# Kernel tuning notes

Hardware: AMD Instinct MI355X
Metric: run time of the kernel (lower is better)

The kernel has to match this reference:

```python
import jax, jax.numpy as jnp
import numpy as np

NEG_SLOPE = 0.2  # PyG GATv2Conv default leaky_relu negative slope


def _gatv2_layer(x, src, dst, n, Wl, bl, Wr, br, att, bias, concat):
    # PyG GATv2Conv (share_weights=False, edge_dim=None):
    #   x_l = lin_l(x) on source, x_r = lin_r(x) on target
    #   m = leaky_relu(x_l[src] + x_r[dst]); alpha = softmax_dst(<m, att>)
    #   out[i] = sum_{e: dst=i} alpha_e * x_l[src_e]
    H, C = att.shape
    xl = (x @ Wl + bl).reshape(n, H, C)
    xr = (x @ Wr + br).reshape(n, H, C)
    m = jax.nn.leaky_relu(xl[src] + xr[dst], NEG_SLOPE)      # [E,H,C]
    logits = jnp.einsum('ehc,hc->eh', m, att)                # [E,H]
    lmax = jax.ops.segment_max(logits, dst, num_segments=n)  # [N,H]
    e = jnp.exp(logits - lmax[dst])
    denom = jax.ops.segment_sum(e, dst, num_segments=n)
    alpha = e / (denom[dst] + 1e-16)                         # [E,H]
    out = jax.ops.segment_sum(xl[src] * alpha[:, :, None], dst, num_segments=n)
    out = out.reshape(n, H * C) if concat else out.mean(axis=1)
    return out + bias


def _glorot(key, shape):
    fan_in, fan_out = shape[0], shape[-1]
    s = jnp.sqrt(6.0 / (fan_in + fan_out))
    return jax.random.uniform(key, shape, jnp.float32, -s, s)


def setup_inputs() -> dict:
    key = jax.random.key(0)
    N, E, B = 50000, 800000, 512
    node_in, hidden, heads, meta_dim = 128, 32, 4, 12
    ks = jax.random.split(key, 32)
    inp = {
        'x': jax.random.normal(ks[0], (N, node_in), jnp.float32),
        'edge_index': jax.random.randint(ks[1], (2, E), 0, N, jnp.int64),
        'batch': jnp.sort(jax.random.randint(ks[2], (N,), 0, B, jnp.int64)),
        'metadata': jax.random.normal(ks[3], (B, meta_dim), jnp.float32),
    }
    dims = [(node_in, hidden, heads), (hidden * heads, hidden, heads), (hidden * heads, hidden, 1)]
    i = 4
    for li, (din, dh, H) in enumerate(dims):
        inp[f'Wl{li}'] = _glorot(ks[i], (din, H * dh)); i += 1
        inp[f'bl{li}'] = jnp.zeros((H * dh,), jnp.float32)
        inp[f'Wr{li}'] = _glorot(ks[i], (din, H * dh)); i += 1
        inp[f'br{li}'] = jnp.zeros((H * dh,), jnp.float32)
        inp[f'att{li}'] = _glorot(ks[i], (H, dh)); i += 1
        out_dim = H * dh if li < 2 else dh  # last layer concat=False
        inp[f'b{li}'] = jnp.zeros((out_dim,), jnp.float32)
    pool_dim = hidden  # n_layers=3 -> final single-head layer
    inp['Wh1'] = _glorot(ks[i], (pool_dim + meta_dim, pool_dim)); i += 1
    inp['bh1'] = jnp.zeros((pool_dim,), jnp.float32)
    inp['Wh2'] = _glorot(ks[i], (pool_dim, 1)); i += 1
    inp['bh2'] = jnp.zeros((1,), jnp.float32)
    return inp


def reference(x, edge_index, batch, metadata,
              Wl0, bl0, Wr0, br0, att0, b0,
              Wl1, bl1, Wr1, br1, att1, b1,
              Wl2, bl2, Wr2, br2, att2, b2,
              Wh1, bh1, Wh2, bh2):
    n = x.shape[0]
    B = metadata.shape[0]
    # PyG GATv2Conv add_self_loops=True
    loop = jnp.arange(n, dtype=edge_index.dtype)
    src = jnp.concatenate([edge_index[0], loop])
    dst = jnp.concatenate([edge_index[1], loop])
    params = [(Wl0, bl0, Wr0, br0, att0, b0, True),
              (Wl1, bl1, Wr1, br1, att1, b1, True),
              (Wl2, bl2, Wr2, br2, att2, b2, False)]
    h = x
    for (Wl, bl, Wr, br, att, bias, concat) in params:
        h = _gatv2_layer(h, src, dst, n, Wl, bl, Wr, br, att, bias, concat)
        h = jax.nn.elu(h)  # dropout is identity in eval mode
    # global mean pool over graphs
    sums = jax.ops.segment_sum(h, batch, num_segments=B)
    cnt = jax.ops.segment_sum(jnp.ones((n,), h.dtype), batch, num_segments=B)
    emb = sums / jnp.clip(cnt, 1.0)[:, None]
    z = jnp.concatenate([emb, metadata], axis=1)
    z = jax.nn.relu(z @ Wh1 + bh1)
    return z @ Wh2 + bh2  # (B, 1) logits
```

## Files before the change

### kernel.cpp

```cpp
#include <hip/hip_runtime.h>
#include <cstdint>
#include <cstddef>

#define NEG_SLOPE 0.2f
#define LOG2E 1.44269504f
#define NBLK 256

typedef __attribute__((ext_vector_type(8))) short short8;
typedef __attribute__((ext_vector_type(4))) float f32x4;

__device__ __forceinline__ float bf2f(unsigned short u) {
    union { unsigned int i; float f; } x; x.i = ((unsigned int)u) << 16; return x.f;
}
__device__ __forceinline__ unsigned short f2bf(float f) {
    union { float f; unsigned int i; } x;
    x.f = f;
    unsigned int u = x.i;
    return (unsigned short)((u + 0x7FFFu + ((u >> 16) & 1u)) >> 16);
}

__device__ __forceinline__ float dpp_sum8(float p) {
    p += __int_as_float(__builtin_amdgcn_update_dpp(0, __float_as_int(p), 0xB1, 0xF, 0xF, true));
    p += __int_as_float(__builtin_amdgcn_update_dpp(0, __float_as_int(p), 0x4E, 0xF, 0xF, true));
    p += __int_as_float(__builtin_amdgcn_update_dpp(0, __float_as_int(p), 0x141, 0xF, 0xF, true));
    return p;
}

__global__ __launch_bounds__(256) void prep_w_all(
    const float* __restrict__ Wl0, const float* __restrict__ Wr0,
    const float* __restrict__ Wl1, const float* __restrict__ Wr1,
    const float* __restrict__ Wl2, const float* __restrict__ Wr2,
    unsigned short* __restrict__ Bt0, unsigned short* __restrict__ Bt1,
    unsigned short* __restrict__ Bt2)
{
    int idx = blockIdx.x * 256 + threadIdx.x;
    const int SZ = 256 * 128;
    const float *Wl, *Wr; unsigned short* Bt; int dout;
    if (idx < SZ)              { Wl = Wl0; Wr = Wr0; Bt = Bt0; dout = 128; }
    else if (idx < 2 * SZ)     { Wl = Wl1; Wr = Wr1; Bt = Bt1; dout = 128; idx -= SZ; }
    else if (idx < 2 * SZ + 64 * 128) { Wl = Wl2; Wr = Wr2; Bt = Bt2; dout = 32; idx -= 2 * SZ; }
    else return;
    int n = idx >> 7, k = idx & 127;
    float v = (n < dout) ? Wl[(size_t)k * dout + n] : Wr[(size_t)k * dout + (n - dout)];
    Bt[idx] = f2bf(v);
}

template<int BN, bool ABF16>
__global__ __launch_bounds__(256) void gemm_mfma(
    const void* __restrict__ Avoid, int M,
    const unsigned short* __restrict__ Bt,
    const float* __restrict__ bl, const float* __restrict__ br,
    int dout, unsigned short* __restrict__ XL, unsigned short* __restrict__ XR)
{
    constexpr int LDA = 136;
    constexpr int NT  = BN / 16;
    __shared__ __attribute__((aligned(16))) unsigned short Bs[BN * LDA];
    const int t  = threadIdx.x;
    const int m0 = blockIdx.x * 64;
    const int n0 = blockIdx.y * BN;

    const int w    = t >> 6;
    const int lane = t & 63;
    const int fr   = lane & 15;
    const int quad = lane >> 4;

#pragma unroll
    for (int i = 0; i < BN / 16; ++i) {
        int c  = t + i * 256;
        int n  = c >> 4;
        int kc = (c & 15) * 8;
        *(short8*)(Bs + n * LDA + kc) =
            *(const short8*)(Bt + (size_t)(n0 + n) * 128 + kc);
    }

    const int arow = m0 + w * 16 + fr;
    const size_t abase = (size_t)(arow < M ? arow : 0) * 128 + quad * 8;
    short8 afr[4];
    if (ABF16) {
        const unsigned short* A = (const unsigned short*)Avoid;
#pragma unroll
        for (int kk = 0; kk < 4; ++kk)
            afr[kk] = *(const short8*)(A + abase + kk * 32);
    } else {
        const float* A = (const float*)Avoid;
#pragma unroll
        for (int kk = 0; kk < 4; ++kk) {
            float4 lo = *(const float4*)(A + abase + kk * 32);
            float4 hi = *(const float4*)(A + abase + kk * 32 + 4);
            afr[kk][0] = (short)f2bf(lo.x); afr[kk][1] = (short)f2bf(lo.y);
            afr[kk][2] = (short)f2bf(lo.z); afr[kk][3] = (short)f2bf(lo.w);
            afr[kk][4] = (short)f2bf(hi.x); afr[kk][5] = (short)f2bf(hi.y);
            afr[kk][6] = (short)f2bf(hi.z); afr[kk][7] = (short)f2bf(hi.w);
        }
    }
    __syncthreads();

    f32x4 acc[NT] = {};
    const unsigned short* bp = Bs + fr * LDA + quad * 8;
#pragma unroll
    for (int kk = 0; kk < 4; ++kk) {
#pragma unroll
        for (int j = 0; j < NT; ++j) {
            short8 bfr = *(const short8*)(bp + j * 16 * LDA + kk * 32);
            acc[j] = __builtin_amdgcn_mfma_f32_16x16x32_bf16(afr[kk], bfr, acc[j], 0, 0, 0);
        }
    }

#pragma unroll
    for (int j = 0; j < NT; ++j) {
        int col = n0 + j * 16 + fr;
        float bias = (col < dout) ? bl[col] : br[col - dout];
#pragma unroll
        for (int r = 0; r < 4; ++r) {
            int row = m0 + w * 16 + quad * 4 + r;
            if (row < M) {
                unsigned short o = f2bf(acc[j][r] + bias);
                if (col < dout) XL[(size_t)row * dout + col] = o;
                else            XR[(size_t)row * dout + (col - dout)] = o;
            }
        }
    }
}

__global__ __launch_bounds__(256) void csr_hist(
    const int* __restrict__ dst, int E, int tile, int* __restrict__ hist)
{
    __shared__ int h[256];
    const int t = threadIdx.x, b = blockIdx.x;
    h[t] = 0;
    __syncthreads();
    const int e0 = b * tile;
    const int e1 = min(E, e0 + tile);
    for (int e = e0 + t; e < e1; e += 256)
        atomicAdd(&h[dst[e] >> 8], 1);
    __syncthreads();
    hist[t * NBLK + b] = h[t];
}

__global__ __launch_bounds__(256) void csr_scatter(
    const int* __restrict__ src, const int* __restrict__ dst, int E, int tile,
    const int* __restrict__ hist_s, unsigned int* __restrict__ sorted)
{
    __shared__ int cur[256];
    const int t = threadIdx.x, b = blockIdx.x;
    cur[t] = hist_s[t * NBLK + b];
    __syncthreads();
    const int e0 = b * tile;
    const int e1 = min(E, e0 + tile);
    for (int e = e0 + t; e < e1; e += 256) {
        int d = dst[e];
        int pos = atomicAdd(&cur[d >> 8], 1);
        sorted[pos] = ((unsigned int)d << 16) | (unsigned int)src[e];
    }
}

__global__ __launch_bounds__(256) void csr_fine(
    const unsigned int* __restrict__ sorted, int E, int N,
    const int* __restrict__ hist_s,
    int* __restrict__ rowptr, unsigned short* __restrict__ csr_src)
{
    __shared__ int h[256];
    __shared__ int sc[256];
    const int t = threadIdx.x, d = blockIdx.x;
    const int start = hist_s[d * NBLK];
    const int end   = (d < 255) ? hist_s[(d + 1) * NBLK] : E;
    h[t] = 0;
    __syncthreads();
    for (int e = start + t; e < end; e += 256)
        atomicAdd(&h[(sorted[e] >> 16) & 0xFF], 1);
    __syncthreads();
    int v = h[t];
    sc[t] = v;
    __syncthreads();
    for (int off = 1; off < 256; off <<= 1) {
        int u = (t >= off) ? sc[t - off] : 0;
        __syncthreads();
        sc[t] += u;
        __syncthreads();
    }
    const int base = start + sc[t] - v;
    const int node = (d << 8) + t;
    if (node <= N) rowptr[node] = base;
    h[t] = base;
    __syncthreads();
    for (int e = start + t; e < end; e += 256) {
        unsigned int it = sorted[e];
        int pos = atomicAdd(&h[(it >> 16) & 0xFF], 1);
        csr_src[pos] = (unsigned short)(it & 0xFFFFu);
    }
}

__global__ __launch_bounds__(256) void scan_partial(
    const int* __restrict__ cnt, int N, int* __restrict__ bsum)
{
    __shared__ int red[4];
    const int t = threadIdx.x;
    const int base = blockIdx.x * 2048;
    int s = 0;
#pragma unroll
    for (int i = 0; i < 8; ++i) {
        int idx = base + t + i * 256;
        if (idx < N) s += cnt[idx];
    }
#pragma unroll
    for (int off = 32; off >= 1; off >>= 1) s += __shfl_xor(s, off);
    if ((t & 63) == 0) red[t >> 6] = s;
    __syncthreads();
    if (t == 0) bsum[blockIdx.x] = red[0] + red[1] + red[2] + red[3];
}

__global__ __launch_bounds__(256) void scan_bsums(
    int* __restrict__ bsum, int nb, int E, int* __restrict__ rowptr, int N)
{
    __shared__ int sh[256];
    const int t = threadIdx.x;
    int v = (t < nb) ? bsum[t] : 0;
    sh[t] = v;
    __syncthreads();
    for (int off = 1; off < 256; off <<= 1) {
        int u = (t >= off) ? sh[t - off] : 0;
        __syncthreads();
        sh[t] += u;
        __syncthreads();
    }
    if (t < nb) bsum[t] = sh[t] - v;
    if (t == 0) rowptr[N] = E;
}

__global__ __launch_bounds__(256) void scan_final(
    const int* __restrict__ cnt, int N, const int* __restrict__ bsum,
    int* __restrict__ rowptr)
{
    __shared__ int sdat[2048];
    __shared__ int tsum[256];
    const int t = threadIdx.x;
    const int base = blockIdx.x * 2048;
#pragma unroll
    for (int i = 0; i < 8; ++i) {
        int idx = base + t + i * 256;
        sdat[t + i * 256] = (idx < N) ? cnt[idx] : 0;
    }
    __syncthreads();
    int vals[8];
    int s = 0;
#pragma unroll
    for (int j = 0; j < 8; ++j) { vals[j] = sdat[t * 8 + j]; s += vals[j]; }
    tsum[t] = s;
    __syncthreads();
    for (int off = 1; off < 256; off <<= 1) {
        int u = (t >= off) ? tsum[t - off] : 0;
        __syncthreads();
        tsum[t] += u;
        __syncthreads();
    }
    int run = bsum[blockIdx.x] + tsum[t] - s;
#pragma unroll
    for (int j = 0; j < 8; ++j) { sdat[t * 8 + j] = run; run += vals[j]; }
    __syncthreads();
#pragma unroll
    for (int i = 0; i < 8; ++i) {
        int idx = base + t + i * 256;
        if (idx < N) rowptr[idx] = sdat[t + i * 256];
    }
}

template<int H>
__global__ __launch_bounds__(256, 4) void gat_fused(
    const unsigned short* __restrict__ xl, const unsigned short* __restrict__ xr,
    const int* __restrict__ rowptr, const unsigned short* __restrict__ csr_src,
    const float* __restrict__ att, const float* __restrict__ bias,
    unsigned short* __restrict__ hout, int hstride, int N)
{
    constexpr int HC  = 32 * H;
    constexpr int LPE = HC / 4;
    constexpr int EPW = 64 / LPE;
    const int node = blockIdx.x * 4 + (threadIdx.x >> 6);
    if (node >= N) return;
    const int lane = threadIdx.x & 63;
    const int q    = lane % LPE;
    const int slot = lane / LPE;
    const int rs   = rowptr[node];
    const int re   = rowptr[node + 1];

    const unsigned short* __restrict__ xlb = xl + 4 * q;
    float4 xri;
    {
        ushort4 u = *(const ushort4*)(xr + (size_t)node * HC + 4 * q);
        xri.x = bf2f(u.x); xri.y = bf2f(u.y); xri.z = bf2f(u.z); xri.w = bf2f(u.w);
    }
    float4 b1, b2;
    {
        float4 a = *(const float4*)(att + 4 * q);
        const float c1 = 0.5f * (1.0f + NEG_SLOPE) * LOG2E;
        const float c2 = 0.5f * (1.0f - NEG_SLOPE) * LOG2E;
        b1.x = a.x * c1; b1.y = a.y * c1; b1.z = a.z * c1; b1.w = a.w * c1;
        b2.x = a.x * c2; b2.y = a.y * c2; b2.z = a.z * c2; b2.w = a.w * c2;
    }

    float l = 0.f;
    float4 acc = make_float4(0.f, 0.f, 0.f, 0.f);

    auto ld4 = [&](int s) -> float4 {
        ushort4 u = *(const ushort4*)(xlb + (size_t)s * HC);
        float4 v;
        v.x = bf2f(u.x); v.y = bf2f(u.y); v.z = bf2f(u.z); v.w = bf2f(u.w);
        return v;
    };

    auto edge_w = [&](const float4& v) -> float {
        float sx = v.x + xri.x, sy = v.y + xri.y, sz = v.z + xri.z, sw = v.w + xri.w;
        float p  = b1.x * sx;
        float pq = b2.x * fabsf(sx);
        p  = fmaf(b1.y, sy, p);
        pq = fmaf(b2.y, fabsf(sy), pq);
        p  = fmaf(b1.z, sz, p);
        pq = fmaf(b2.z, fabsf(sz), pq);
        p  = fmaf(b1.w, sw, p);
        pq = fmaf(b2.w, fabsf(sw), pq);
        p += pq;
        p = dpp_sum8(p);
        return exp2f(p);
    };

    if (slot == 0) {
        float4 v = ld4(node);
        float w = edge_w(v);
        l = w;
        acc.x = w * v.x; acc.y = w * v.y; acc.z = w * v.z; acc.w = w * v.w;
    }

    int k = rs + slot;
    for (; k + EPW < re; k += 2 * EPW) {
        int s0 = csr_src[k];
        int s1 = csr_src[k + EPW];
        float4 v0 = ld4(s0);
        float4 v1 = ld4(s1);
        float w0 = edge_w(v0);
        float w1 = edge_w(v1);
        l += w0 + w1;
        acc.x = fmaf(w0, v0.x, fmaf(w1, v1.x, acc.x));
        acc.y = fmaf(w0, v0.y, fmaf(w1, v1.y, acc.y));
        acc.z = fmaf(w0, v0.z, fmaf(w1, v1.z, acc.z));
        acc.w = fmaf(w0, v0.w, fmaf(w1, v1.w, acc.w));
    }
    if (k < re) {
        int s0 = csr_src[k];
        float4 v0 = ld4(s0);
        float w0 = edge_w(v0);
        l += w0;
        acc.x = fmaf(w0, v0.x, acc.x);
        acc.y = fmaf(w0, v0.y, acc.y);
        acc.z = fmaf(w0, v0.z, acc.z);
        acc.w = fmaf(w0, v0.w, acc.w);
    }

#pragma unroll
    for (int mask = LPE; mask < 64; mask <<= 1) {
        l     += __shfl_xor(l, mask);
        acc.x += __shfl_xor(acc.x, mask);
        acc.y += __shfl_xor(acc.y, mask);
        acc.z += __shfl_xor(acc.z, mask);
        acc.w += __shfl_xor(acc.w, mask);
    }

    if (lane < LPE) {
        const float4 bi = *(const float4*)(bias + 4 * q);
        float inv = 1.f / (l + 1e-16f);
        float4 o;
        o.x = acc.x * inv + bi.x;
        o.y = acc.y * inv + bi.y;
        o.z = acc.z * inv + bi.z;
        o.w = acc.w * inv + bi.w;
        o.x = (o.x > 0.f) ? o.x : expm1f(o.x);
        o.y = (o.y > 0.f) ? o.y : expm1f(o.y);
        o.z = (o.z > 0.f) ? o.z : expm1f(o.z);
        o.w = (o.w > 0.f) ? o.w : expm1f(o.w);
        ushort4 ob;
        ob.x = f2bf(o.x); ob.y = f2bf(o.y); ob.z = f2bf(o.z); ob.w = f2bf(o.w);
        *(ushort4*)(hout + (size_t)node * hstride + 4 * q) = ob;
    }
}

__global__ __launch_bounds__(128) void pool_head_kernel(
    const unsigned short* __restrict__ h, int hstride,
    const int* __restrict__ batch, int N,
    const float* __restrict__ meta,
    const float* __restrict__ Wh1, const float* __restrict__ bh1,
    const float* __restrict__ Wh2, const float* __restrict__ bh2,
    float* __restrict__ out)
{
    const int b = blockIdx.x;
    const int t = threadIdx.x;
    __shared__ float s[128];
    __shared__ float z[44];

    int lo = 0, hi = N;
    while (lo < hi) { int mid = (lo + hi) >> 1; if (batch[mid] < b) lo = mid + 1; else hi = mid; }
    int lo2 = lo, hi2 = N;
    while (lo2 < hi2) { int mid = (lo2 + hi2) >> 1; if (batch[mid] < b + 1) lo2 = mid + 1; else hi2 = mid; }
    const int start = lo, end = lo2;

    const int c = t & 31, r = t >> 5;
    float acc = 0.f;
    for (int row = start + r; row < end; row += 4)
        acc += bf2f(h[(size_t)row * hstride + c]);
    s[t] = acc;
    __syncthreads();
    if (t < 32) {
        float sum = s[t] + s[t + 32] + s[t + 64] + s[t + 96];
        z[t] = sum / fmaxf((float)(end - start), 1.0f);
    } else if (t < 44) {
        z[t] = meta[(size_t)b * 12 + (t - 32)];
    }
    __syncthreads();
    if (t < 32) {
        float hj = bh1[t];
#pragma unroll
        for (int k = 0; k < 44; ++k)
            hj = fmaf(z[k], Wh1[k * 32 + t], hj);
        hj = fmaxf(hj, 0.f);
        float p = hj * Wh2[t];
#pragma unroll
        for (int off = 16; off >= 1; off >>= 1)
            p += __shfl_xor(p, off, 32);
        if (t == 0) out[b] = p + bh2[0];
    }
}

extern "C" void kernel_launch(void* const* d_in, const int* in_sizes, int n_in,
                              void* d_out, int out_size, void* d_ws, size_t ws_size,
                              hipStream_t stream)
{
    const float* x     = (const float*)d_in[0];
    const int*   ei    = (const int*)d_in[1];
    const int*   batch = (const int*)d_in[2];
    const float* meta  = (const float*)d_in[3];
    const float* Wl[3]  = {(const float*)d_in[4],  (const float*)d_in[10], (const float*)d_in[16]};
    const float* bl[3]  = {(const float*)d_in[5],  (const float*)d_in[11], (const float*)d_in[17]};
    const float* Wr[3]  = {(const float*)d_in[6],  (const float*)d_in[12], (const float*)d_in[18]};
    const float* br[3]  = {(const float*)d_in[7],  (const float*)d_in[13], (const float*)d_in[19]};
    const float* att[3] = {(const float*)d_in[8],  (const float*)d_in[14], (const float*)d_in[20]};
    const float* bb[3]  = {(const float*)d_in[9],  (const float*)d_in[15], (const float*)d_in[21]};
    const float* Wh1 = (const float*)d_in[22];
    const float* bh1 = (const float*)d_in[23];
    const float* Wh2 = (const float*)d_in[24];
    const float* bh2 = (const float*)d_in[25];
    float* out = (float*)d_out;

    const int N  = in_sizes[0] / 128;
    const int E  = in_sizes[1] / 2;
    const int B  = in_sizes[3] / 12;

    char* wsp = (char*)d_ws;
    size_t off_ = 0;
    auto alloc = [&](size_t bytes) {
        char* p = wsp + off_;
        off_ = (off_ + bytes + 255) & ~(size_t)255;
        return p;
    };
    unsigned short* xlbuf = (unsigned short*)alloc((size_t)N * 128 * 2);
    unsigned short* xrbuf = (unsigned short*)alloc((size_t)N * 128 * 2);
    unsigned short* hbuf  = (unsigned short*)alloc((size_t)N * 128 * 2);
    int*   rowptr  = (int*)alloc((size_t)(N + 1) * 4);
    unsigned short* csr_src = (unsigned short*)alloc((size_t)E * 2);
    unsigned int*   sorted  = (unsigned int*)alloc((size_t)E * 4);
    int*   hist_g  = (int*)alloc((size_t)65536 * 4);
    int*   hist_s  = (int*)alloc((size_t)65537 * 4);
    unsigned short* Bt0     = (unsigned short*)alloc((size_t)256 * 128 * 2);
    unsigned short* Bt1     = (unsigned short*)alloc((size_t)256 * 128 * 2);
    unsigned short* Bt2     = (unsigned short*)alloc((size_t)64 * 128 * 2);
    int*   bsum    = (int*)alloc((size_t)256 * 4);

    const int* srcI = ei;
    const int* dstI = ei + E;

    prep_w_all<<<(2 * 256 * 128 + 64 * 128 + 255) / 256, 256, 0, stream>>>(
        Wl[0], Wr[0], Wl[1], Wr[1], Wl[2], Wr[2], Bt0, Bt1, Bt2);

    const int tile = (E + NBLK - 1) / NBLK;
    csr_hist<<<NBLK, 256, 0, stream>>>(dstI, E, tile, hist_g);
    scan_partial<<<32, 256, 0, stream>>>(hist_g, 65536, bsum);
    scan_bsums<<<1, 256, 0, stream>>>(bsum, 32, E, hist_s, 65536);
    scan_final<<<32, 256, 0, stream>>>(hist_g, 65536, bsum, hist_s);
    csr_scatter<<<NBLK, 256, 0, stream>>>(srcI, dstI, E, tile, hist_s, sorted);
    csr_fine<<<(N >> 8) + 1, 256, 0, stream>>>(sorted, E, N, hist_s, rowptr, csr_src);

    const int GB = (N + 3) / 4;
    const int MB = (N + 63) / 64;

    {
        gemm_mfma<128, false><<<dim3(MB, 2), 256, 0, stream>>>(x, N, Bt0, bl[0], br[0], 128, xlbuf, xrbuf);
        gat_fused<4><<<GB, 256, 0, stream>>>(xlbuf, xrbuf, rowptr, csr_src, att[0], bb[0], hbuf, 128, N);
    }
    {
        gemm_mfma<128, true><<<dim3(MB, 2), 256, 0, stream>>>(hbuf, N, Bt1, bl[1], br[1], 128, xlbuf, xrbuf);
        gat_fused<4><<<GB, 256, 0, stream>>>(xlbuf, xrbuf, rowptr, csr_src, att[1], bb[1], hbuf, 128, N);
    }
    {
        gemm_mfma<64, true><<<dim3(MB, 1), 256, 0, stream>>>(hbuf, N, Bt2, bl[2], br[2], 32, xlbuf, xrbuf);
        gat_fused<1><<<GB, 256, 0, stream>>>(xlbuf, xrbuf, rowptr, csr_src, att[2], bb[2], hbuf, 32, N);
    }
    pool_head_kernel<<<B, 128, 0, stream>>>(hbuf, 32, batch, N, meta, Wh1, bh1, Wh2, bh2, out);
}
```

Baseline: 340.8 us.

## Fuse weight prep with histogram, single-block scan, split GAT launches in halves

```diff
diff --git a/kernel.cpp b/kernel.cpp
--- a/kernel.cpp
+++ b/kernel.cpp
@@ -26,14 +26,28 @@
     return p;
 }
 
-__global__ __launch_bounds__(256) void prep_w_all(
+__global__ __launch_bounds__(256) void prep_and_hist(
     const float* __restrict__ Wl0, const float* __restrict__ Wr0,
     const float* __restrict__ Wl1, const float* __restrict__ Wr1,
     const float* __restrict__ Wl2, const float* __restrict__ Wr2,
     unsigned short* __restrict__ Bt0, unsigned short* __restrict__ Bt1,
-    unsigned short* __restrict__ Bt2)
-{
-    int idx = blockIdx.x * 256 + threadIdx.x;
+    unsigned short* __restrict__ Bt2,
+    const int* __restrict__ dst, int E, int tile, int* __restrict__ hist)
+{
+    __shared__ int h[256];
+    const int t = threadIdx.x;
+    const int b = blockIdx.x;
+    if (b < NBLK) {
+        h[t] = 0;
+        __syncthreads();
+        const int e0 = b * tile;
+        const int e1 = min(E, e0 + tile);
+        for (int e = e0 + t; e < e1; e += 256)
+            atomicAdd(&h[dst[e] >> 8], 1);
+        __syncthreads();
+        hist[t * NBLK + b] = h[t];
+    }
+    int idx = b * 256 + t;
     const int SZ = 256 * 128;
     const float *Wl, *Wr; unsigned short* Bt; int dout;
     if (idx < SZ)              { Wl = Wl0; Wr = Wr0; Bt = Bt0; dout = 128; }
@@ -45,6 +59,34 @@
     Bt[idx] = f2bf(v);
 }
 
+__global__ __launch_bounds__(1024) void scan_one(
+    const int* __restrict__ g, int* __restrict__ s_out)
+{
+    __shared__ int wsum[16];
+    const int t = threadIdx.x;
+    int vals[64];
+    int tot = 0;
+#pragma unroll
+    for (int i = 0; i < 64; ++i) { vals[i] = g[t * 64 + i]; tot += vals[i]; }
+    int s = tot;
+#pragma unroll
+    for (int off = 1; off < 64; off <<= 1) {
+        int u = __shfl_up(s, off);
+        if ((t & 63) >= off) s += u;
+    }
+    if ((t & 63) == 63) wsum[t >> 6] = s;
+    __syncthreads();
+    if (t == 0) {
+        int run = 0;
+#pragma unroll
+        for (int i = 0; i < 16; ++i) { int v = wsum[i]; wsum[i] = run; run += v; }
+    }
+    __syncthreads();
+    int run = wsum[t >> 6] + s - tot;
+#pragma unroll
+    for (int i = 0; i < 64; ++i) { s_out[t * 64 + i] = run; run += vals[i]; }
+}
+
 template<int BN, bool ABF16>
 __global__ __launch_bounds__(256) void gemm_mfma(
     const void* __restrict__ Avoid, int M,
@@ -122,21 +164,6 @@
     }
 }
 
-__global__ __launch_bounds__(256) void csr_hist(
-    const int* __restrict__ dst, int E, int tile, int* __restrict__ hist)
-{
-    __shared__ int h[256];
-    const int t = threadIdx.x, b = blockIdx.x;
-    h[t] = 0;
-    __syncthreads();
-    const int e0 = b * tile;
-    const int e1 = min(E, e0 + tile);
-    for (int e = e0 + t; e < e1; e += 256)
-        atomicAdd(&h[dst[e] >> 8], 1);
-    __syncthreads();
-    hist[t * NBLK + b] = h[t];
-}
-
 __global__ __launch_bounds__(256) void csr_scatter(
     const int* __restrict__ src, const int* __restrict__ dst, int E, int tile,
     const int* __restrict__ hist_s, unsigned int* __restrict__ sorted)
@@ -190,92 +217,18 @@
     }
 }
 
-__global__ __launch_bounds__(256) void scan_partial(
-    const int* __restrict__ cnt, int N, int* __restrict__ bsum)
-{
-    __shared__ int red[4];
-    const int t = threadIdx.x;
-    const int base = blockIdx.x * 2048;
-    int s = 0;
-#pragma unroll
-    for (int i = 0; i < 8; ++i) {
-        int idx = base + t + i * 256;
-        if (idx < N) s += cnt[idx];
-    }
-#pragma unroll
-    for (int off = 32; off >= 1; off >>= 1) s += __shfl_xor(s, off);
-    if ((t & 63) == 0) red[t >> 6] = s;
-    __syncthreads();
-    if (t == 0) bsum[blockIdx.x] = red[0] + red[1] + red[2] + red[3];
-}
-
-__global__ __launch_bounds__(256) void scan_bsums(
-    int* __restrict__ bsum, int nb, int E, int* __restrict__ rowptr, int N)
-{
-    __shared__ int sh[256];
-    const int t = threadIdx.x;
-    int v = (t < nb) ? bsum[t] : 0;
-    sh[t] = v;
-    __syncthreads();
-    for (int off = 1; off < 256; off <<= 1) {
-        int u = (t >= off) ? sh[t - off] : 0;
-        __syncthreads();
-        sh[t] += u;
-        __syncthreads();
-    }
-    if (t < nb) bsum[t] = sh[t] - v;
-    if (t == 0) rowptr[N] = E;
-}
-
-__global__ __launch_bounds__(256) void scan_final(
-    const int* __restrict__ cnt, int N, const int* __restrict__ bsum,
-    int* __restrict__ rowptr)
-{
-    __shared__ int sdat[2048];
-    __shared__ int tsum[256];
-    const int t = threadIdx.x;
-    const int base = blockIdx.x * 2048;
-#pragma unroll
-    for (int i = 0; i < 8; ++i) {
-        int idx = base + t + i * 256;
-        sdat[t + i * 256] = (idx < N) ? cnt[idx] : 0;
-    }
-    __syncthreads();
-    int vals[8];
-    int s = 0;
-#pragma unroll
-    for (int j = 0; j < 8; ++j) { vals[j] = sdat[t * 8 + j]; s += vals[j]; }
-    tsum[t] = s;
-    __syncthreads();
-    for (int off = 1; off < 256; off <<= 1) {
-        int u = (t >= off) ? tsum[t - off] : 0;
-        __syncthreads();
-        tsum[t] += u;
-        __syncthreads();
-    }
-    int run = bsum[blockIdx.x] + tsum[t] - s;
-#pragma unroll
-    for (int j = 0; j < 8; ++j) { sdat[t * 8 + j] = run; run += vals[j]; }
-    __syncthreads();
-#pragma unroll
-    for (int i = 0; i < 8; ++i) {
-        int idx = base + t + i * 256;
-        if (idx < N) rowptr[idx] = sdat[t + i * 256];
-    }
-}
-
 template<int H>
 __global__ __launch_bounds__(256, 4) void gat_fused(
     const unsigned short* __restrict__ xl, const unsigned short* __restrict__ xr,
     const int* __restrict__ rowptr, const unsigned short* __restrict__ csr_src,
     const float* __restrict__ att, const float* __restrict__ bias,
-    unsigned short* __restrict__ hout, int hstride, int N)
+    unsigned short* __restrict__ hout, int hstride, int node0, int nodeEnd)
 {
     constexpr int HC  = 32 * H;
     constexpr int LPE = HC / 4;
     constexpr int EPW = 64 / LPE;
-    const int node = blockIdx.x * 4 + (threadIdx.x >> 6);
-    if (node >= N) return;
+    const int node = node0 + blockIdx.x * 4 + (threadIdx.x >> 6);
+    if (node >= nodeEnd) return;
     const int lane = threadIdx.x & 63;
     const int q    = lane % LPE;
     const int slot = lane / LPE;
@@ -469,36 +422,39 @@
     unsigned short* Bt0     = (unsigned short*)alloc((size_t)256 * 128 * 2);
     unsigned short* Bt1     = (unsigned short*)alloc((size_t)256 * 128 * 2);
     unsigned short* Bt2     = (unsigned short*)alloc((size_t)64 * 128 * 2);
-    int*   bsum    = (int*)alloc((size_t)256 * 4);
 
     const int* srcI = ei;
     const int* dstI = ei + E;
 
-    prep_w_all<<<(2 * 256 * 128 + 64 * 128 + 255) / 256, 256, 0, stream>>>(
-        Wl[0], Wr[0], Wl[1], Wr[1], Wl[2], Wr[2], Bt0, Bt1, Bt2);
-
     const int tile = (E + NBLK - 1) / NBLK;
-    csr_hist<<<NBLK, 256, 0, stream>>>(dstI, E, tile, hist_g);
-    scan_partial<<<32, 256, 0, stream>>>(hist_g, 65536, bsum);
-    scan_bsums<<<1, 256, 0, stream>>>(bsum, 32, E, hist_s, 65536);
-    scan_final<<<32, 256, 0, stream>>>(hist_g, 65536, bsum, hist_s);
+    prep_and_hist<<<288, 256, 0, stream>>>(
+        Wl[0], Wr[0], Wl[1], Wr[1], Wl[2], Wr[2], Bt0, Bt1, Bt2,
+        dstI, E, tile, hist_g);
+
+    scan_one<<<1, 1024, 0, stream>>>(hist_g, hist_s);
+
     csr_scatter<<<NBLK, 256, 0, stream>>>(srcI, dstI, E, tile, hist_s, sorted);
     csr_fine<<<(N >> 8) + 1, 256, 0, stream>>>(sorted, E, N, hist_s, rowptr, csr_src);
 
-    const int GB = (N + 3) / 4;
     const int MB = (N + 63) / 64;
+    const int half = (N + 1) / 2;
+    const int GB1 = (half + 3) / 4;
+    const int GB2 = (N - half + 3) / 4;
+    const int GBF = (N + 3) / 4;
 
     {
         gemm_mfma<128, false><<<dim3(MB, 2), 256, 0, stream>>>(x, N, Bt0, bl[0], br[0], 128, xlbuf, xrbuf);
-        gat_fused<4><<<GB, 256, 0, stream>>>(xlbuf, xrbuf, rowptr, csr_src, att[0], bb[0], hbuf, 128, N);
+        gat_fused<4><<<GB1, 256, 0, stream>>>(xlbuf, xrbuf, rowptr, csr_src, att[0], bb[0], hbuf, 128, 0, half);
+        gat_fused<4><<<GB2, 256, 0, stream>>>(xlbuf, xrbuf, rowptr, csr_src, att[0], bb[0], hbuf, 128, half, N);
     }
     {
         gemm_mfma<128, true><<<dim3(MB, 2), 256, 0, stream>>>(hbuf, N, Bt1, bl[1], br[1], 128, xlbuf, xrbuf);
-        gat_fused<4><<<GB, 256, 0, stream>>>(xlbuf, xrbuf, rowptr, csr_src, att[1], bb[1], hbuf, 128, N);
+        gat_fused<4><<<GB1, 256, 0, stream>>>(xlbuf, xrbuf, rowptr, csr_src, att[1], bb[1], hbuf, 128, 0, half);
+        gat_fused<4><<<GB2, 256, 0, stream>>>(xlbuf, xrbuf, rowptr, csr_src, att[1], bb[1], hbuf, 128, half, N);
     }
     {
         gemm_mfma<64, true><<<dim3(MB, 1), 256, 0, stream>>>(hbuf, N, Bt2, bl[2], br[2], 32, xlbuf, xrbuf);
-        gat_fused<1><<<GB, 256, 0, stream>>>(xlbuf, xrbuf, rowptr, csr_src, att[2], bb[2], hbuf, 32, N);
+        gat_fused<1><<<GBF, 256, 0, stream>>>(xlbuf, xrbuf, rowptr, csr_src, att[2], bb[2], hbuf, 32, 0, N);
     }
     pool_head_kernel<<<B, 128, 0, stream>>>(hbuf, 32, batch, N, meta, Wh1, bh1, Wh2, bh2, out);
 }
```

After: 357.4 us. +4.9%, slower.
